# Kernel optimization log

Hardware: AMD Instinct MI355X
Metric: run time of the kernel (lower is better)

Reference implementation:

```python
import jax, jax.numpy as jnp
import numpy as np

N, M, D = 384, 2, 3          # n_nodes, multiplicity, spatial dim
F, H, K, L = 32, 64, 2, 2    # feat dim, hidden, n_equivariant_vectors_out, n_blocks
OUT = 64                     # n_invariant_feat_out
T = N * M                    # flattened node count

def _edges():
    # fully-connected graph over flattened nodes, no self edges (static shapes)
    idx = np.arange(T)
    s = np.repeat(idx, T)
    r = np.tile(idx, T)
    mask = s != r
    return jnp.asarray(s[mask]), jnp.asarray(r[mask])

def setup_inputs() -> dict:
    key = jax.random.key(0)
    ks = jax.random.split(key, 12)
    def w(k, shape):
        return (jax.random.normal(k, shape) / np.sqrt(shape[-2])).astype(jnp.float32)
    return {
        "positions": jax.random.normal(ks[0], (N, M, D), dtype=jnp.float32),
        "features": jax.random.normal(ks[1], (N, M, F), dtype=jnp.float32),
        "w_emb": w(ks[2], (F, H)), "b_emb": jnp.zeros((H,), jnp.float32),
        "we1": w(ks[3], (L, 2 * H + K, H)), "be1": jnp.zeros((L, H), jnp.float32),
        "we2": w(ks[4], (L, H, H)), "be2": jnp.zeros((L, H), jnp.float32),
        "wx1": w(ks[5], (L, H, H)), "bx1": jnp.zeros((L, H), jnp.float32),
        "wx2": w(ks[6], (L, H, K)),
        "wh1": w(ks[7], (L, 2 * H, H)), "bh1": jnp.zeros((L, H), jnp.float32),
        "wh2": w(ks[8], (L, H, H)), "bh2": jnp.zeros((L, H), jnp.float32),
        "w_head": w(ks[9], (H, OUT)), "b_head": jnp.zeros((OUT,), jnp.float32),
    }

def reference(positions, features, w_emb, b_emb, we1, be1, we2, be2,
              wx1, bx1, wx2, wh1, bh1, wh2, bh2, w_head, b_head):
    senders, receivers = _edges()
    x = positions.reshape(T, D)                      # flatten multiplicity
    h = features.reshape(T, F) @ w_emb + b_emb       # [T,H] node embedding
    x_vec = jnp.repeat(x[:, None, :], K, axis=1)     # [T,K,3] vector channels
    for l in range(L):
        diff = x_vec[senders] - x_vec[receivers]                        # [E,K,3]
        sqnorm = jnp.sum(diff * diff, axis=-1)                          # [E,K]
        e_in = jnp.concatenate([h[senders], h[receivers], sqnorm], -1)  # [E,2H+K]
        m = jax.nn.silu(e_in @ we1[l] + be1[l])
        m = jax.nn.silu(m @ we2[l] + be2[l])                            # [E,H]
        phi_x = jax.nn.silu(m @ wx1[l] + bx1[l]) @ wx2[l]               # [E,K]
        upd = phi_x[..., None] * diff / (jnp.sqrt(sqnorm + 1e-8)[..., None] + 1.0)
        x_vec = x_vec + jax.ops.segment_sum(upd, receivers, num_segments=T) / (T - 1)
        agg = jax.ops.segment_sum(m, receivers, num_segments=T)         # [T,H]
        h = h + jax.nn.silu(jnp.concatenate([h, agg], -1) @ wh1[l] + bh1[l]) @ wh2[l] + bh2[l]
    vectors = (x_vec - x[:, None, :]).reshape(N, M, K, D)  # unflatten
    scalars = (h @ w_head + b_head).reshape(N, M, OUT)     # invariant head
    return vectors, scalars
```

## Files before the change

kernel.cpp:

```cpp
#include <hip/hip_runtime.h>
#include <math.h>

#define TN 768
#define HD 64
#define FF 32
#define OUTD 64
#define LL 2

typedef short short8 __attribute__((ext_vector_type(8)));
typedef short short4v __attribute__((ext_vector_type(4)));
typedef float f32x4 __attribute__((ext_vector_type(4)));
typedef unsigned int uint4v __attribute__((ext_vector_type(4)));

__device__ __forceinline__ float silu_f(float x) {
    float e = __builtin_amdgcn_exp2f(x * -1.44269504089f);
    return x * __builtin_amdgcn_rcpf(1.0f + e);
}

__device__ __forceinline__ void bf16_split(float x, short& hi, short& lo) {
    unsigned int u = __float_as_uint(x);
    unsigned int uh = u & 0xFFFF0000u;
    hi = (short)(uh >> 16);
    float r = x - __uint_as_float(uh);
    lo = (short)(__float_as_uint(r) >> 16);
}

__device__ __forceinline__ unsigned short bf16_rne(float x) {
    unsigned int u = __float_as_uint(x);
    u += 0x7FFFu + ((u >> 16) & 1u);
    return (unsigned short)(u >> 16);
}

__device__ __forceinline__ unsigned int pk_bf16(float a, float b) {
#if __has_builtin(__builtin_amdgcn_cvt_pk_bf16_f32)
    auto t = __builtin_amdgcn_cvt_pk_bf16_f32(a, b);
    return __builtin_bit_cast(unsigned int, t);
#else
    unsigned int ua = __float_as_uint(a); ua += 0x7FFFu + ((ua >> 16) & 1u);
    unsigned int ub = __float_as_uint(b); ub += 0x7FFFu + ((ub >> 16) & 1u);
    return __builtin_amdgcn_perm(ub, ua, 0x07060302u);
#endif
}

__device__ __forceinline__ float row16_sum(float v) {
    int x;
    x = __builtin_amdgcn_update_dpp(0, __float_as_int(v), 0xB1, 0xF, 0xF, true);
    v += __int_as_float(x);
    x = __builtin_amdgcn_update_dpp(0, __float_as_int(v), 0x4E, 0xF, 0xF, true);
    v += __int_as_float(x);
    x = __builtin_amdgcn_update_dpp(0, __float_as_int(v), 0x141, 0xF, 0xF, true);
    v += __int_as_float(x);
    x = __builtin_amdgcn_update_dpp(0, __float_as_int(v), 0x140, 0xF, 0xF, true);
    v += __int_as_float(x);
    return v;
}

__global__ void k_embed_pre(const float* __restrict__ pos, const float* __restrict__ feat,
                            const float* __restrict__ w_emb, const float* __restrict__ b_emb,
                            const float* __restrict__ we1, const float* __restrict__ be1,
                            float* __restrict__ h, float* __restrict__ x_vec,
                            float* __restrict__ A, float* __restrict__ Bv) {
    int t = blockIdx.x;
    int j = threadIdx.x;
    __shared__ float sf[FF];
    __shared__ float sh[HD];
    if (j < FF) sf[j] = feat[t * FF + j];
    __syncthreads();
    float acc = b_emb[j];
#pragma unroll
    for (int f = 0; f < FF; ++f) acc += sf[f] * w_emb[f * HD + j];
    h[t * HD + j] = acc;
    sh[j] = acc;
    if (j < 6) x_vec[t * 6 + j] = pos[t * 3 + (j % 3)];
    __syncthreads();
    float a = be1[j], b = 0.f;
#pragma unroll
    for (int i = 0; i < HD; ++i) {
        a += sh[i] * we1[i * HD + j];
        b += sh[i] * we1[(HD + i) * HD + j];
    }
    A[t * HD + j] = a;
    Bv[t * HD + j] = b;
}

#define SM2S 68
__global__ __launch_bounds__(256, 1) void k_edge(
    const float* __restrict__ xv_in, const float* __restrict__ A_in,
    const float* __restrict__ Bv_in, const float* __restrict__ we1,
    const float* __restrict__ we2, const float* __restrict__ be2,
    const float* __restrict__ wx1, const float* __restrict__ bx1,
    const float* __restrict__ wx2,
    const float* __restrict__ wh1, const float* __restrict__ bh1,
    const float* __restrict__ wh2, const float* __restrict__ bh2,
    const float* __restrict__ be1,
    float* __restrict__ h, float* __restrict__ xv_out,
    float* __restrict__ A_out, float* __restrict__ Bv_out,
    const float* __restrict__ pos, const float* __restrict__ w_head,
    const float* __restrict__ b_head, float* __restrict__ out,
    int l, int last)
{
    const int r = blockIdx.x;
    const int tid = threadIdx.x;
    const int wv = tid >> 6;
    const int lane = tid & 63;
    const int q = lane >> 4;
    const int m = lane & 15;

    __shared__ __align__(16) union USm {
        struct {
            unsigned short W2h[64 * 72], W2l[64 * 72], W3h[64 * 72];
        } stg;
        struct {
            unsigned short M2[64 * SM2S];
            float Phi[64][2];
            float Agg[4][64];
            float XupW[4][8];
            float hr[64], aggF[64], su[64], h2[64];
        } run;
    } u;

    const float* w2 = we2 + (size_t)l * HD * HD;
    const float* w3 = wx1 + (size_t)l * HD * HD;
    for (int e = tid; e < HD * HD; e += 256) {
        int k = e >> 6, n = e & 63;
        short h16, l16;
        bf16_split(w2[e], h16, l16);
        u.stg.W2h[n * 72 + k] = (unsigned short)h16;
        u.stg.W2l[n * 72 + k] = (unsigned short)l16;
        u.stg.W3h[n * 72 + k] = bf16_rne(w3[e]);
    }
    __syncthreads();
    short8 bW2h[4][2], bW2l[4][2], bW3h[4][2];
#pragma unroll
    for (int nt = 0; nt < 4; ++nt)
#pragma unroll
        for (int kt = 0; kt < 2; ++kt) {
            int idx = (nt * 16 + m) * 72 + kt * 32 + 8 * q;
            bW2h[nt][kt] = *(const short8*)&u.stg.W2h[idx];
            bW2l[nt][kt] = *(const short8*)&u.stg.W2l[idx];
            bW3h[nt][kt] = *(const short8*)&u.stg.W3h[idx];
        }
    __syncthreads();

    float bbA[2][8], c0A[2][8], c1A[2][8];
#pragma unroll
    for (int kt = 0; kt < 2; ++kt) {
        int jb = kt * 32 + 8 * q;
        *(float4*)&bbA[kt][0] = *(const float4*)&Bv_in[r * HD + jb];
        *(float4*)&bbA[kt][4] = *(const float4*)&Bv_in[r * HD + jb + 4];
        *(float4*)&c0A[kt][0] = *(const float4*)&we1[((size_t)l * 130 + 128) * HD + jb];
        *(float4*)&c0A[kt][4] = *(const float4*)&we1[((size_t)l * 130 + 128) * HD + jb + 4];
        *(float4*)&c1A[kt][0] = *(const float4*)&we1[((size_t)l * 130 + 129) * HD + jb];
        *(float4*)&c1A[kt][4] = *(const float4*)&we1[((size_t)l * 130 + 129) * HD + jb + 4];
    }
    float be2v[4], bx1v[4], w20[4], w21[4];
#pragma unroll
    for (int nt = 0; nt < 4; ++nt) {
        int col = nt * 16 + m;
        be2v[nt] = be2[l * HD + col];
        bx1v[nt] = bx1[l * HD + col];
        w20[nt] = wx2[((size_t)l * HD + col) * 2 + 0];
        w21[nt] = wx2[((size_t)l * HD + col) * 2 + 1];
    }
    float xr[6];
#pragma unroll
    for (int c = 0; c < 6; ++c) xr[c] = xv_in[r * 6 + c];

    float aggP[4] = {0.f, 0.f, 0.f, 0.f};
    float accX[6] = {0.f, 0.f, 0.f, 0.f, 0.f, 0.f};
    const int rowA = 16 * wv + m;

#pragma unroll 1
    for (int s0 = 0; s0 < TN; s0 += 64) {
        const int sA = s0 + rowA;
        float2 p01 = *(const float2*)&xv_in[sA * 6 + 0];
        float2 p23 = *(const float2*)&xv_in[sA * 6 + 2];
        float2 p45 = *(const float2*)&xv_in[sA * 6 + 4];
        float d0 = p01.x - xr[0], d1 = p01.y - xr[1], d2 = p23.x - xr[2];
        float d3 = p23.y - xr[3], d4 = p45.x - xr[4], d5 = p45.y - xr[5];
        float q0 = d0 * d0 + d1 * d1 + d2 * d2;
        float q1 = d3 * d3 + d4 * d4 + d5 * d5;
        float ik0 = __builtin_amdgcn_rcpf(__builtin_amdgcn_sqrtf(q0 + 1e-8f) + 1.f);
        float ik1 = __builtin_amdgcn_rcpf(__builtin_amdgcn_sqrtf(q1 + 1e-8f) + 1.f);

        short8 a1h[2];
#pragma unroll
        for (int kt = 0; kt < 2; ++kt) {
            int jb = kt * 32 + 8 * q;
            float av[8];
            *(float4*)&av[0] = *(const float4*)&A_in[sA * HD + jb];
            *(float4*)&av[4] = *(const float4*)&A_in[sA * HD + jb + 4];
            float mv[8];
#pragma unroll
            for (int jj = 0; jj < 8; ++jj) {
                float pre = av[jj] + bbA[kt][jj] + q0 * c0A[kt][jj] + q1 * c1A[kt][jj];
                mv[jj] = silu_f(pre);
            }
            uint4v uh;
            unsigned int* uhp = (unsigned int*)&uh;
#pragma unroll
            for (int jp = 0; jp < 4; ++jp)
                uhp[jp] = pk_bf16(mv[2 * jp], mv[2 * jp + 1]);
            a1h[kt] = __builtin_bit_cast(short8, uh);
        }

        const int rl = r - s0;
        const bool selfw = (rl >= 16 * wv) && (rl < 16 * wv + 16);
#pragma unroll
        for (int nt = 0; nt < 4; ++nt) {
            f32x4 acc = {0.f, 0.f, 0.f, 0.f};
#pragma unroll
            for (int kt = 0; kt < 2; ++kt) {
                acc = __builtin_amdgcn_mfma_f32_16x16x32_bf16(a1h[kt], bW2h[nt][kt], acc, 0, 0, 0);
                acc = __builtin_amdgcn_mfma_f32_16x16x32_bf16(a1h[kt], bW2l[nt][kt], acc, 0, 0, 0);
            }
            float vv[4];
#pragma unroll
            for (int reg = 0; reg < 4; ++reg) vv[reg] = silu_f(acc[reg] + be2v[nt]);
            const int il0 = 16 * wv + 4 * q;
            if (__builtin_expect(selfw, 0)) {
#pragma unroll
                for (int reg = 0; reg < 4; ++reg)
                    aggP[nt] += (il0 + reg == rl) ? 0.f : vv[reg];
            } else {
#pragma unroll
                for (int reg = 0; reg < 4; ++reg) aggP[nt] += vv[reg];
            }
            const int col = nt * 16 + m;
            unsigned int pA = pk_bf16(vv[0], vv[1]);
            unsigned int pB = pk_bf16(vv[2], vv[3]);
            u.run.M2[(il0 + 0) * SM2S + col] = (unsigned short)pA;
            u.run.M2[(il0 + 1) * SM2S + col] = (unsigned short)(pA >> 16);
            u.run.M2[(il0 + 2) * SM2S + col] = (unsigned short)pB;
            u.run.M2[(il0 + 3) * SM2S + col] = (unsigned short)(pB >> 16);
        }

        short8 a2h[2];
#pragma unroll
        for (int kt = 0; kt < 2; ++kt) {
            int base = rowA * SM2S + kt * 32 + 8 * q;
            short4v lo = *(const short4v*)&u.run.M2[base];
            short4v hi = *(const short4v*)&u.run.M2[base + 4];
            short8 a2;
#pragma unroll
            for (int jj = 0; jj < 4; ++jj) { a2[jj] = lo[jj]; a2[4 + jj] = hi[jj]; }
            a2h[kt] = a2;
        }
        float phiP[4][2] = {};
#pragma unroll
        for (int nt = 0; nt < 4; ++nt) {
            f32x4 acc = {0.f, 0.f, 0.f, 0.f};
#pragma unroll
            for (int kt = 0; kt < 2; ++kt)
                acc = __builtin_amdgcn_mfma_f32_16x16x32_bf16(a2h[kt], bW3h[nt][kt], acc, 0, 0, 0);
#pragma unroll
            for (int reg = 0; reg < 4; ++reg) {
                float p = silu_f(acc[reg] + bx1v[nt]);
                phiP[reg][0] += p * w20[nt];
                phiP[reg][1] += p * w21[nt];
            }
        }
#pragma unroll
        for (int reg = 0; reg < 4; ++reg) {
            phiP[reg][0] = row16_sum(phiP[reg][0]);
            phiP[reg][1] = row16_sum(phiP[reg][1]);
        }
        if (m == 0) {
#pragma unroll
            for (int reg = 0; reg < 4; ++reg) {
                int il = 16 * wv + 4 * q + reg;
                *(float2*)&u.run.Phi[il][0] = make_float2(phiP[reg][0], phiP[reg][1]);
            }
        }
        if (q == 0) {
            float2 ph = *(const float2*)&u.run.Phi[rowA][0];
            float f0 = ph.x * ik0;
            float f1 = ph.y * ik1;
            accX[0] += f0 * d0; accX[1] += f0 * d1; accX[2] += f0 * d2;
            accX[3] += f1 * d3; accX[4] += f1 * d4; accX[5] += f1 * d5;
        }
    }

#pragma unroll
    for (int nt = 0; nt < 4; ++nt) {
        aggP[nt] += __shfl_xor(aggP[nt], 16, 64);
        aggP[nt] += __shfl_xor(aggP[nt], 32, 64);
    }
#pragma unroll
    for (int c = 0; c < 6; ++c) accX[c] = row16_sum(accX[c]);
    if (q == 0) {
#pragma unroll
        for (int nt = 0; nt < 4; ++nt) u.run.Agg[wv][nt * 16 + m] = aggP[nt];
        if (m == 0) {
#pragma unroll
            for (int c = 0; c < 6; ++c) u.run.XupW[wv][c] = accX[c];
        }
    }
    __syncthreads();

    float xup = 0.f;
    if (tid < 64) {
        u.run.aggF[tid] = u.run.Agg[0][tid] + u.run.Agg[1][tid] +
                          u.run.Agg[2][tid] + u.run.Agg[3][tid];
        u.run.hr[tid] = h[r * HD + tid];
    }
    __syncthreads();
    if (tid < 64) {
        int j = tid;
        const float* w1 = wh1 + (size_t)l * 128 * HD;
        float acc = bh1[l * HD + j];
#pragma unroll
        for (int i = 0; i < HD; ++i) acc += u.run.hr[i] * w1[i * HD + j];
#pragma unroll
        for (int i = 0; i < HD; ++i) acc += u.run.aggF[i] * w1[(HD + i) * HD + j];
        u.run.su[j] = silu_f(acc);
    }
    __syncthreads();
    if (tid < 64) {
        int j = tid;
        const float* wq = wh2 + (size_t)l * HD * HD;
        float v = 0.f;
#pragma unroll
        for (int i = 0; i < HD; ++i) v += u.run.su[i] * wq[i * HD + j];
        float hn = u.run.hr[j] + v + bh2[l * HD + j];
        h[r * HD + j] = hn;
        u.run.h2[j] = hn;
    }
    if (tid < 6) {
        xup = u.run.XupW[0][tid] + u.run.XupW[1][tid] +
              u.run.XupW[2][tid] + u.run.XupW[3][tid];
    }
    __syncthreads();
    if (!last) {
        if (tid < 64) {
            int j = tid;
            const float* w = we1 + (size_t)(l + 1) * 130 * HD;
            float a = be1[(l + 1) * HD + j], b = 0.f;
#pragma unroll
            for (int i = 0; i < HD; ++i) {
                a += u.run.h2[i] * w[i * HD + j];
                b += u.run.h2[i] * w[(HD + i) * HD + j];
            }
            A_out[r * HD + j] = a;
            Bv_out[r * HD + j] = b;
        }
        if (tid < 6) {
            xv_out[r * 6 + tid] = xr[tid] + xup * (1.0f / 767.0f);
        }
    } else {
        if (tid < 64) {
            int j = tid;
            float o = b_head[j];
#pragma unroll
            for (int i = 0; i < HD; ++i) o += u.run.h2[i] * w_head[i * OUTD + j];
            out[TN * 6 + r * OUTD + j] = o;
        }
        if (tid < 6) {
            float xv = xr[tid] + xup * (1.0f / 767.0f);
            out[r * 6 + tid] = xv - pos[r * 3 + (tid % 3)];
        }
    }
}

extern "C" void kernel_launch(void* const* d_in, const int* in_sizes, int n_in,
                              void* d_out, int out_size, void* d_ws, size_t ws_size,
                              hipStream_t stream)
{
    const float* pos    = (const float*)d_in[0];
    const float* feat   = (const float*)d_in[1];
    const float* w_emb  = (const float*)d_in[2];
    const float* b_emb  = (const float*)d_in[3];
    const float* we1    = (const float*)d_in[4];
    const float* be1    = (const float*)d_in[5];
    const float* we2    = (const float*)d_in[6];
    const float* be2    = (const float*)d_in[7];
    const float* wx1    = (const float*)d_in[8];
    const float* bx1    = (const float*)d_in[9];
    const float* wx2    = (const float*)d_in[10];
    const float* wh1    = (const float*)d_in[11];
    const float* bh1    = (const float*)d_in[12];
    const float* wh2    = (const float*)d_in[13];
    const float* bh2    = (const float*)d_in[14];
    const float* w_head = (const float*)d_in[15];
    const float* b_head = (const float*)d_in[16];
    float* out = (float*)d_out;

    float* ws   = (float*)d_ws;
    float* h    = ws;
    float* xv0  = h + TN * HD;
    float* xv1  = xv0 + TN * 6;
    float* A0   = xv1 + TN * 6;
    float* A1   = A0 + TN * HD;
    float* Bv0  = A1 + TN * HD;
    float* Bv1  = Bv0 + TN * HD;

    k_embed_pre<<<TN, 64, 0, stream>>>(pos, feat, w_emb, b_emb, we1, be1,
                                       h, xv0, A0, Bv0);
    k_edge<<<TN, 256, 0, stream>>>(xv0, A0, Bv0, we1, we2, be2, wx1, bx1, wx2,
                                   wh1, bh1, wh2, bh2, be1,
                                   h, xv1, A1, Bv1,
                                   pos, w_head, b_head, out, 0, 0);
    k_edge<<<TN, 256, 0, stream>>>(xv1, A1, Bv1, we1, we2, be2, wx1, bx1, wx2,
                                   wh1, bh1, wh2, bh2, be1,
                                   h, xv0, A0, Bv0,
                                   pos, w_head, b_head, out, 1, 1);
}
```

Measured before the change: 210.5 us.

## Split edge kernel across two sender halves and move node update to separate kernel

The edge kernel now launches two blocks per receiver, each covering half of the sender tiles and writing partial aggregates and coordinate updates to a workspace. A new small node kernel sums the two partials and runs the node MLP, the next layer's A/B precompute, and the head. The wx1 bf16 weights stay in shared memory and are reloaded per tile instead of held in registers, which lowers register pressure. This doubles the grid to improve occupancy and load balance on the many-CU device, at the cost of two extra kernel launches, extra global traffic for partials, and duplicated per-block weight staging.

```diff
diff --git a/kernel.cpp b/kernel.cpp
--- a/kernel.cpp
+++ b/kernel.cpp
@@ -90,32 +90,28 @@
     const float* __restrict__ we2, const float* __restrict__ be2,
     const float* __restrict__ wx1, const float* __restrict__ bx1,
     const float* __restrict__ wx2,
-    const float* __restrict__ wh1, const float* __restrict__ bh1,
-    const float* __restrict__ wh2, const float* __restrict__ bh2,
-    const float* __restrict__ be1,
-    float* __restrict__ h, float* __restrict__ xv_out,
-    float* __restrict__ A_out, float* __restrict__ Bv_out,
-    const float* __restrict__ pos, const float* __restrict__ w_head,
-    const float* __restrict__ b_head, float* __restrict__ out,
-    int l, int last)
+    float* __restrict__ Pagg,
+    float* __restrict__ Pxup,
+    int l)
 {
-    const int r = blockIdx.x;
+    const int r = blockIdx.x >> 1;
+    const int half = blockIdx.x & 1;
     const int tid = threadIdx.x;
     const int wv = tid >> 6;
     const int lane = tid & 63;
     const int q = lane >> 4;
     const int m = lane & 15;
 
+    __shared__ __align__(16) unsigned short sW3[64 * 72];
     __shared__ __align__(16) union USm {
         struct {
-            unsigned short W2h[64 * 72], W2l[64 * 72], W3h[64 * 72];
+            unsigned short W2h[64 * 72], W2l[64 * 72];
         } stg;
         struct {
             unsigned short M2[64 * SM2S];
             float Phi[64][2];
             float Agg[4][64];
             float XupW[4][8];
-            float hr[64], aggF[64], su[64], h2[64];
         } run;
     } u;
 
@@ -127,10 +123,10 @@
         bf16_split(w2[e], h16, l16);
         u.stg.W2h[n * 72 + k] = (unsigned short)h16;
         u.stg.W2l[n * 72 + k] = (unsigned short)l16;
-        u.stg.W3h[n * 72 + k] = bf16_rne(w3[e]);
-    }
-    __syncthreads();
-    short8 bW2h[4][2], bW2l[4][2], bW3h[4][2];
+        sW3[n * 72 + k] = bf16_rne(w3[e]);
+    }
+    __syncthreads();
+    short8 bW2h[4][2], bW2l[4][2];
 #pragma unroll
     for (int nt = 0; nt < 4; ++nt)
 #pragma unroll
@@ -138,7 +134,6 @@
             int idx = (nt * 16 + m) * 72 + kt * 32 + 8 * q;
             bW2h[nt][kt] = *(const short8*)&u.stg.W2h[idx];
             bW2l[nt][kt] = *(const short8*)&u.stg.W2l[idx];
-            bW3h[nt][kt] = *(const short8*)&u.stg.W3h[idx];
         }
     __syncthreads();
 
@@ -171,7 +166,8 @@
     const int rowA = 16 * wv + m;
 
 #pragma unroll 1
-    for (int s0 = 0; s0 < TN; s0 += 64) {
+    for (int it = half; it < TN / 64; it += 2) {
+        const int s0 = it * 64;
         const int sA = s0 + rowA;
         float2 p01 = *(const float2*)&xv_in[sA * 6 + 0];
         float2 p23 = *(const float2*)&xv_in[sA * 6 + 2];
@@ -251,8 +247,11 @@
         for (int nt = 0; nt < 4; ++nt) {
             f32x4 acc = {0.f, 0.f, 0.f, 0.f};
 #pragma unroll
-            for (int kt = 0; kt < 2; ++kt)
-                acc = __builtin_amdgcn_mfma_f32_16x16x32_bf16(a2h[kt], bW3h[nt][kt], acc, 0, 0, 0);
+            for (int kt = 0; kt < 2; ++kt) {
+                int widx = (nt * 16 + m) * 72 + kt * 32 + 8 * q;
+                short8 wh = *(const short8*)&sW3[widx];
+                acc = __builtin_amdgcn_mfma_f32_16x16x32_bf16(a2h[kt], wh, acc, 0, 0, 0);
+            }
 #pragma unroll
             for (int reg = 0; reg < 4; ++reg) {
                 float p = silu_f(acc[reg] + bx1v[nt]);
@@ -297,68 +296,72 @@
         }
     }
     __syncthreads();
-
-    float xup = 0.f;
     if (tid < 64) {
-        u.run.aggF[tid] = u.run.Agg[0][tid] + u.run.Agg[1][tid] +
-                          u.run.Agg[2][tid] + u.run.Agg[3][tid];
-        u.run.hr[tid] = h[r * HD + tid];
-    }
-    __syncthreads();
-    if (tid < 64) {
-        int j = tid;
-        const float* w1 = wh1 + (size_t)l * 128 * HD;
-        float acc = bh1[l * HD + j];
-#pragma unroll
-        for (int i = 0; i < HD; ++i) acc += u.run.hr[i] * w1[i * HD + j];
-#pragma unroll
-        for (int i = 0; i < HD; ++i) acc += u.run.aggF[i] * w1[(HD + i) * HD + j];
-        u.run.su[j] = silu_f(acc);
-    }
-    __syncthreads();
-    if (tid < 64) {
-        int j = tid;
-        const float* wq = wh2 + (size_t)l * HD * HD;
-        float v = 0.f;
-#pragma unroll
-        for (int i = 0; i < HD; ++i) v += u.run.su[i] * wq[i * HD + j];
-        float hn = u.run.hr[j] + v + bh2[l * HD + j];
-        h[r * HD + j] = hn;
-        u.run.h2[j] = hn;
-    }
-    if (tid < 6) {
-        xup = u.run.XupW[0][tid] + u.run.XupW[1][tid] +
-              u.run.XupW[2][tid] + u.run.XupW[3][tid];
+        float s = u.run.Agg[0][tid] + u.run.Agg[1][tid] +
+                  u.run.Agg[2][tid] + u.run.Agg[3][tid];
+        Pagg[((size_t)half * TN + r) * HD + tid] = s;
+    } else if (tid >= 64 && tid < 70) {
+        int c = tid - 64;
+        float s = u.run.XupW[0][c] + u.run.XupW[1][c] +
+                  u.run.XupW[2][c] + u.run.XupW[3][c];
+        Pxup[((size_t)half * TN + r) * 8 + c] = s;
+    }
+}
+
+__global__ void k_node(float* __restrict__ h,
+                       const float* __restrict__ Pagg, const float* __restrict__ Pxup,
+                       const float* __restrict__ wh1, const float* __restrict__ bh1,
+                       const float* __restrict__ wh2, const float* __restrict__ bh2,
+                       float* __restrict__ xv,
+                       const float* __restrict__ we1, const float* __restrict__ be1,
+                       float* __restrict__ A, float* __restrict__ Bv,
+                       const float* __restrict__ pos, const float* __restrict__ w_head,
+                       const float* __restrict__ b_head, float* __restrict__ out,
+                       int l, int last)
+{
+    int r = blockIdx.x;
+    int j = threadIdx.x;
+    __shared__ float hr[HD], ag[HD], su[HD], h2[HD];
+    hr[j] = h[r * HD + j];
+    ag[j] = Pagg[r * HD + j] + Pagg[(size_t)TN * HD + r * HD + j];
+    __syncthreads();
+    const float* w1 = wh1 + (size_t)l * 128 * HD;
+    float acc = bh1[l * HD + j];
+#pragma unroll
+    for (int i = 0; i < HD; ++i) acc += hr[i] * w1[i * HD + j];
+#pragma unroll
+    for (int i = 0; i < HD; ++i) acc += ag[i] * w1[(HD + i) * HD + j];
+    su[j] = silu_f(acc);
+    __syncthreads();
+    const float* wq = wh2 + (size_t)l * HD * HD;
+    float v = 0.f;
+#pragma unroll
+    for (int i = 0; i < HD; ++i) v += su[i] * wq[i * HD + j];
+    float hn = hr[j] + v + bh2[l * HD + j];
+    h[r * HD + j] = hn;
+    h2[j] = hn;
+    if (j < 6) {
+        float xu = Pxup[r * 8 + j] + Pxup[(size_t)TN * 8 + r * 8 + j];
+        float x = xv[r * 6 + j] + xu * (1.0f / 767.0f);
+        xv[r * 6 + j] = x;
+        if (last) out[r * 6 + j] = x - pos[r * 3 + (j % 3)];
     }
     __syncthreads();
     if (!last) {
-        if (tid < 64) {
-            int j = tid;
-            const float* w = we1 + (size_t)(l + 1) * 130 * HD;
-            float a = be1[(l + 1) * HD + j], b = 0.f;
-#pragma unroll
-            for (int i = 0; i < HD; ++i) {
-                a += u.run.h2[i] * w[i * HD + j];
-                b += u.run.h2[i] * w[(HD + i) * HD + j];
-            }
-            A_out[r * HD + j] = a;
-            Bv_out[r * HD + j] = b;
-        }
-        if (tid < 6) {
-            xv_out[r * 6 + tid] = xr[tid] + xup * (1.0f / 767.0f);
-        }
+        const float* w = we1 + (size_t)(l + 1) * 130 * HD;
+        float a = be1[(l + 1) * HD + j], b = 0.f;
+#pragma unroll
+        for (int i = 0; i < HD; ++i) {
+            a += h2[i] * w[i * HD + j];
+            b += h2[i] * w[(HD + i) * HD + j];
+        }
+        A[r * HD + j] = a;
+        Bv[r * HD + j] = b;
     } else {
-        if (tid < 64) {
-            int j = tid;
-            float o = b_head[j];
-#pragma unroll
-            for (int i = 0; i < HD; ++i) o += u.run.h2[i] * w_head[i * OUTD + j];
-            out[TN * 6 + r * OUTD + j] = o;
-        }
-        if (tid < 6) {
-            float xv = xr[tid] + xup * (1.0f / 767.0f);
-            out[r * 6 + tid] = xv - pos[r * 3 + (tid % 3)];
-        }
+        float o = b_head[j];
+#pragma unroll
+        for (int i = 0; i < HD; ++i) o += h2[i] * w_head[i * OUTD + j];
+        out[TN * 6 + r * OUTD + j] = o;
     }
 }
 
@@ -387,21 +390,19 @@
 
     float* ws   = (float*)d_ws;
     float* h    = ws;
-    float* xv0  = h + TN * HD;
-    float* xv1  = xv0 + TN * 6;
-    float* A0   = xv1 + TN * 6;
-    float* A1   = A0 + TN * HD;
-    float* Bv0  = A1 + TN * HD;
-    float* Bv1  = Bv0 + TN * HD;
+    float* xv   = h + TN * HD;
+    float* A    = xv + TN * 6;
+    float* Bv   = A + TN * HD;
+    float* Pagg = Bv + TN * HD;
+    float* Pxup = Pagg + 2 * TN * HD;
 
     k_embed_pre<<<TN, 64, 0, stream>>>(pos, feat, w_emb, b_emb, we1, be1,
-                                       h, xv0, A0, Bv0);
-    k_edge<<<TN, 256, 0, stream>>>(xv0, A0, Bv0, we1, we2, be2, wx1, bx1, wx2,
-                                   wh1, bh1, wh2, bh2, be1,
-                                   h, xv1, A1, Bv1,
-                                   pos, w_head, b_head, out, 0, 0);
-    k_edge<<<TN, 256, 0, stream>>>(xv1, A1, Bv1, we1, we2, be2, wx1, bx1, wx2,
-                                   wh1, bh1, wh2, bh2, be1,
-                                   h, xv0, A0, Bv0,
-                                   pos, w_head, b_head, out, 1, 1);
-}
+                                       h, xv, A, Bv);
+    for (int l = 0; l < LL; ++l) {
+        k_edge<<<2 * TN, 256, 0, stream>>>(xv, A, Bv, we1, we2, be2, wx1, bx1, wx2,
+                                           Pagg, Pxup, l);
+        k_node<<<TN, 64, 0, stream>>>(h, Pagg, Pxup, wh1, bh1, wh2, bh2, xv,
+                                      we1, be1, A, Bv,
+                                      pos, w_head, b_head, out, l, l == LL - 1);
+    }
+}
```

Result: slower. 218.5 us (+3.8%).

## Fuse embed and both edge layers into one cooperative kernel with grid sync

Applied to the files above, without the earlier changes.

Replaces the three launches (embedding plus two edge layers) with a single cooperative kernel that uses grid-wide syncs between stages, with the old three-kernel path kept as a fallback. To let 768 blocks be co-resident (launch bounds raised to 3 blocks per CU), the wx1 weight fragments are no longer held in registers but re-read from shared memory inside the MFMA loop. This is meant to remove launch gaps and tail effects between stages, but adds grid-sync overhead, extra LDS reads and host-side occupancy queries on every call.

```diff
diff --git a/kernel.cpp b/kernel.cpp
--- a/kernel.cpp
+++ b/kernel.cpp
@@ -1,5 +1,8 @@
 #include <hip/hip_runtime.h>
+#include <hip/hip_cooperative_groups.h>
 #include <math.h>
+
+namespace cg = cooperative_groups;
 
 #define TN 768
 #define HD 64
@@ -55,36 +58,22 @@
     return v;
 }
 
-__global__ void k_embed_pre(const float* __restrict__ pos, const float* __restrict__ feat,
-                            const float* __restrict__ w_emb, const float* __restrict__ b_emb,
-                            const float* __restrict__ we1, const float* __restrict__ be1,
-                            float* __restrict__ h, float* __restrict__ x_vec,
-                            float* __restrict__ A, float* __restrict__ Bv) {
-    int t = blockIdx.x;
-    int j = threadIdx.x;
-    __shared__ float sf[FF];
-    __shared__ float sh[HD];
-    if (j < FF) sf[j] = feat[t * FF + j];
-    __syncthreads();
-    float acc = b_emb[j];
-#pragma unroll
-    for (int f = 0; f < FF; ++f) acc += sf[f] * w_emb[f * HD + j];
-    h[t * HD + j] = acc;
-    sh[j] = acc;
-    if (j < 6) x_vec[t * 6 + j] = pos[t * 3 + (j % 3)];
-    __syncthreads();
-    float a = be1[j], b = 0.f;
-#pragma unroll
-    for (int i = 0; i < HD; ++i) {
-        a += sh[i] * we1[i * HD + j];
-        b += sh[i] * we1[(HD + i) * HD + j];
-    }
-    A[t * HD + j] = a;
-    Bv[t * HD + j] = b;
-}
-
 #define SM2S 68
-__global__ __launch_bounds__(256, 1) void k_edge(
+union USm {
+    struct {
+        unsigned short W2h[64 * 72], W2l[64 * 72];
+    } stg;
+    struct {
+        unsigned short M2[64 * SM2S];
+        float Phi[64][2];
+        float Agg[4][64];
+        float XupW[4][8];
+        float hr[64], aggF[64], su[64], h2[64];
+    } run;
+};
+
+__device__ __forceinline__ void layer_body(
+    int r, int tid, USm& u, unsigned short* sW3,
     const float* __restrict__ xv_in, const float* __restrict__ A_in,
     const float* __restrict__ Bv_in, const float* __restrict__ we1,
     const float* __restrict__ we2, const float* __restrict__ be2,
@@ -92,32 +81,16 @@
     const float* __restrict__ wx2,
     const float* __restrict__ wh1, const float* __restrict__ bh1,
     const float* __restrict__ wh2, const float* __restrict__ bh2,
-    const float* __restrict__ be1,
-    float* __restrict__ h, float* __restrict__ xv_out,
-    float* __restrict__ A_out, float* __restrict__ Bv_out,
+    const float* __restrict__ be1, float* __restrict__ h,
+    float* __restrict__ xv_out, float* __restrict__ A_out, float* __restrict__ Bv_out,
     const float* __restrict__ pos, const float* __restrict__ w_head,
     const float* __restrict__ b_head, float* __restrict__ out,
     int l, int last)
 {
-    const int r = blockIdx.x;
-    const int tid = threadIdx.x;
     const int wv = tid >> 6;
     const int lane = tid & 63;
     const int q = lane >> 4;
     const int m = lane & 15;
-
-    __shared__ __align__(16) union USm {
-        struct {
-            unsigned short W2h[64 * 72], W2l[64 * 72], W3h[64 * 72];
-        } stg;
-        struct {
-            unsigned short M2[64 * SM2S];
-            float Phi[64][2];
-            float Agg[4][64];
-            float XupW[4][8];
-            float hr[64], aggF[64], su[64], h2[64];
-        } run;
-    } u;
 
     const float* w2 = we2 + (size_t)l * HD * HD;
     const float* w3 = wx1 + (size_t)l * HD * HD;
@@ -127,10 +100,10 @@
         bf16_split(w2[e], h16, l16);
         u.stg.W2h[n * 72 + k] = (unsigned short)h16;
         u.stg.W2l[n * 72 + k] = (unsigned short)l16;
-        u.stg.W3h[n * 72 + k] = bf16_rne(w3[e]);
-    }
-    __syncthreads();
-    short8 bW2h[4][2], bW2l[4][2], bW3h[4][2];
+        sW3[n * 72 + k] = bf16_rne(w3[e]);
+    }
+    __syncthreads();
+    short8 bW2h[4][2], bW2l[4][2];
 #pragma unroll
     for (int nt = 0; nt < 4; ++nt)
 #pragma unroll
@@ -138,7 +111,6 @@
             int idx = (nt * 16 + m) * 72 + kt * 32 + 8 * q;
             bW2h[nt][kt] = *(const short8*)&u.stg.W2h[idx];
             bW2l[nt][kt] = *(const short8*)&u.stg.W2l[idx];
-            bW3h[nt][kt] = *(const short8*)&u.stg.W3h[idx];
         }
     __syncthreads();
 
@@ -251,8 +223,11 @@
         for (int nt = 0; nt < 4; ++nt) {
             f32x4 acc = {0.f, 0.f, 0.f, 0.f};
 #pragma unroll
-            for (int kt = 0; kt < 2; ++kt)
-                acc = __builtin_amdgcn_mfma_f32_16x16x32_bf16(a2h[kt], bW3h[nt][kt], acc, 0, 0, 0);
+            for (int kt = 0; kt < 2; ++kt) {
+                int widx = (nt * 16 + m) * 72 + kt * 32 + 8 * q;
+                short8 wh = *(const short8*)&sW3[widx];
+                acc = __builtin_amdgcn_mfma_f32_16x16x32_bf16(a2h[kt], wh, acc, 0, 0, 0);
+            }
 #pragma unroll
             for (int reg = 0; reg < 4; ++reg) {
                 float p = silu_f(acc[reg] + bx1v[nt]);
@@ -360,6 +335,115 @@
             out[r * 6 + tid] = xv - pos[r * 3 + (tid % 3)];
         }
     }
+}
+
+__global__ __launch_bounds__(256, 3) void k_fused(
+    const float* __restrict__ pos, const float* __restrict__ feat,
+    const float* __restrict__ w_emb, const float* __restrict__ b_emb,
+    const float* __restrict__ we1, const float* __restrict__ be1,
+    const float* __restrict__ we2, const float* __restrict__ be2,
+    const float* __restrict__ wx1, const float* __restrict__ bx1,
+    const float* __restrict__ wx2,
+    const float* __restrict__ wh1, const float* __restrict__ bh1,
+    const float* __restrict__ wh2, const float* __restrict__ bh2,
+    const float* __restrict__ w_head, const float* __restrict__ b_head,
+    float* __restrict__ out, float* __restrict__ h,
+    float* __restrict__ xv0, float* __restrict__ xv1,
+    float* __restrict__ A0, float* __restrict__ A1,
+    float* __restrict__ Bv0, float* __restrict__ Bv1)
+{
+    cg::grid_group grid = cg::this_grid();
+    const int r = blockIdx.x;
+    const int tid = threadIdx.x;
+    __shared__ __align__(16) USm u;
+    __shared__ __align__(16) unsigned short sW3[64 * 72];
+
+    {
+        float* sf = &u.run.Agg[0][0];
+        float* sh = &u.run.Agg[1][0];
+        if (tid < FF) sf[tid] = feat[r * FF + tid];
+        __syncthreads();
+        if (tid < 64) {
+            float acc = b_emb[tid];
+#pragma unroll
+            for (int f = 0; f < FF; ++f) acc += sf[f] * w_emb[f * HD + tid];
+            h[r * HD + tid] = acc;
+            sh[tid] = acc;
+            if (tid < 6) xv0[r * 6 + tid] = pos[r * 3 + (tid % 3)];
+        }
+        __syncthreads();
+        if (tid < 64) {
+            float a = be1[tid], b = 0.f;
+#pragma unroll
+            for (int i = 0; i < HD; ++i) {
+                a += sh[i] * we1[i * HD + tid];
+                b += sh[i] * we1[(HD + i) * HD + tid];
+            }
+            A0[r * HD + tid] = a;
+            Bv0[r * HD + tid] = b;
+        }
+    }
+    __threadfence();
+    grid.sync();
+
+    layer_body(r, tid, u, sW3, xv0, A0, Bv0, we1, we2, be2, wx1, bx1, wx2,
+               wh1, bh1, wh2, bh2, be1, h, xv1, A1, Bv1,
+               pos, w_head, b_head, out, 0, 0);
+    __threadfence();
+    grid.sync();
+
+    layer_body(r, tid, u, sW3, xv1, A1, Bv1, we1, we2, be2, wx1, bx1, wx2,
+               wh1, bh1, wh2, bh2, be1, h, xv0, A0, Bv0,
+               pos, w_head, b_head, out, 1, 1);
+}
+
+__global__ void k_embed_pre(const float* __restrict__ pos, const float* __restrict__ feat,
+                            const float* __restrict__ w_emb, const float* __restrict__ b_emb,
+                            const float* __restrict__ we1, const float* __restrict__ be1,
+                            float* __restrict__ h, float* __restrict__ x_vec,
+                            float* __restrict__ A, float* __restrict__ Bv) {
+    int t = blockIdx.x;
+    int j = threadIdx.x;
+    __shared__ float sf[FF];
+    __shared__ float sh[HD];
+    if (j < FF) sf[j] = feat[t * FF + j];
+    __syncthreads();
+    float acc = b_emb[j];
+#pragma unroll
+    for (int f = 0; f < FF; ++f) acc += sf[f] * w_emb[f * HD + j];
+    h[t * HD + j] = acc;
+    sh[j] = acc;
+    if (j < 6) x_vec[t * 6 + j] = pos[t * 3 + (j % 3)];
+    __syncthreads();
+    float a = be1[j], b = 0.f;
+#pragma unroll
+    for (int i = 0; i < HD; ++i) {
+        a += sh[i] * we1[i * HD + j];
+        b += sh[i] * we1[(HD + i) * HD + j];
+    }
+    A[t * HD + j] = a;
+    Bv[t * HD + j] = b;
+}
+
+__global__ __launch_bounds__(256, 1) void k_edge_sa(
+    const float* __restrict__ xv_in, const float* __restrict__ A_in,
+    const float* __restrict__ Bv_in, const float* __restrict__ we1,
+    const float* __restrict__ we2, const float* __restrict__ be2,
+    const float* __restrict__ wx1, const float* __restrict__ bx1,
+    const float* __restrict__ wx2,
+    const float* __restrict__ wh1, const float* __restrict__ bh1,
+    const float* __restrict__ wh2, const float* __restrict__ bh2,
+    const float* __restrict__ be1, float* __restrict__ h,
+    float* __restrict__ xv_out, float* __restrict__ A_out, float* __restrict__ Bv_out,
+    const float* __restrict__ pos, const float* __restrict__ w_head,
+    const float* __restrict__ b_head, float* __restrict__ out,
+    int l, int last)
+{
+    __shared__ __align__(16) USm u;
+    __shared__ __align__(16) unsigned short sW3[64 * 72];
+    layer_body(blockIdx.x, threadIdx.x, u, sW3, xv_in, A_in, Bv_in, we1, we2, be2,
+               wx1, bx1, wx2, wh1, bh1, wh2, bh2, be1, h, xv_out, A_out, Bv_out,
+               pos, w_head, b_head, out, l, last);
 }
 
 extern "C" void kernel_launch(void* const* d_in, const int* in_sizes, int n_in,
@@ -394,14 +478,38 @@
     float* Bv0  = A1 + TN * HD;
     float* Bv1  = Bv0 + TN * HD;
 
-    k_embed_pre<<<TN, 64, 0, stream>>>(pos, feat, w_emb, b_emb, we1, be1,
-                                       h, xv0, A0, Bv0);
-    k_edge<<<TN, 256, 0, stream>>>(xv0, A0, Bv0, we1, we2, be2, wx1, bx1, wx2,
-                                   wh1, bh1, wh2, bh2, be1,
-                                   h, xv1, A1, Bv1,
-                                   pos, w_head, b_head, out, 0, 0);
-    k_edge<<<TN, 256, 0, stream>>>(xv1, A1, Bv1, we1, we2, be2, wx1, bx1, wx2,
-                                   wh1, bh1, wh2, bh2, be1,
-                                   h, xv0, A0, Bv0,
-                                   pos, w_head, b_head, out, 1, 1);
-}
+    int dev = 0;
+    hipGetDevice(&dev);
+    int numCU = 0;
+    hipDeviceGetAttribute(&numCU, hipDeviceAttributeMultiprocessorCount, dev);
+    int maxB = 0;
+    hipOccupancyMaxActiveBlocksPerMultiprocessor(&maxB, k_fused, 256, 0);
+
+    bool coop_ok = (maxB > 0 && numCU > 0 && (long)maxB * numCU >= TN);
+    hipError_t err = hipErrorUnknown;
+    if (coop_ok) {
+        void* args[] = {
+            (void*)&pos, (void*)&feat, (void*)&w_emb, (void*)&b_emb,
+            (void*)&we1, (void*)&be1, (void*)&we2, (void*)&be2,
+            (void*)&wx1, (void*)&bx1, (void*)&wx2,
+            (void*)&wh1, (void*)&bh1, (void*)&wh2, (void*)&bh2,
+            (void*)&w_head, (void*)&b_head,
+            (void*)&out, (void*)&h,
+            (void*)&xv0, (void*)&xv1, (void*)&A0, (void*)&A1,
+            (void*)&Bv0, (void*)&Bv1
+        };
+        err = hipLaunchCooperativeKernel(k_fused, dim3(TN), dim3(256), args, 0, stream);
+    }
+    if (!coop_ok || err != hipSuccess) {
+        k_embed_pre<<<TN, 64, 0, stream>>>(pos, feat, w_emb, b_emb, we1, be1,
+                                           h, xv0, A0, Bv0);
+        k_edge_sa<<<TN, 256, 0, stream>>>(xv0, A0, Bv0, we1, we2, be2, wx1, bx1, wx2,
+                                          wh1, bh1, wh2, bh2, be1,
+                                          h, xv1, A1, Bv1,
+                                          pos, w_head, b_head, out, 0, 0);
+        k_edge_sa<<<TN, 256, 0, stream>>>(xv1, A1, Bv1, we1, we2, be2, wx1, bx1, wx2,
+                                          wh1, bh1, wh2, bh2, be1,
+                                          h, xv0, A0, Bv0,
+                                          pos, w_head, b_head, out, 1, 1);
+    }
+}
```

Result: no change. 212.0 us (+0.7%).
